# Kernel tuning notes

Measured on AMD Instinct MI355X. Metric: run time of the kernel, lower is better.

## Reference

```python
import jax, jax.numpy as jnp
import numpy as np

N_KNOTS = 10
NC = 32
BATCH = 32
EPS = 1e-5

def _spline_matrix(n):
    step = 1.0 / (n - 1.0)
    mat = 4 * np.eye(n - 2)
    np.fill_diagonal(mat[1:, :-1], 1)
    np.fill_diagonal(mat[:-1, 1:], 1)
    A = 6 * np.linalg.inv(mat) / step ** 2
    z = np.zeros(n - 2)
    A = np.vstack([z, A, z])            # [n, n-2]
    B = np.zeros((n - 2, n))
    np.fill_diagonal(B, 1)
    np.fill_diagonal(B[:, 1:], -2)
    np.fill_diagonal(B[:, 2:], 1)
    return np.dot(A, B).astype(np.float32)  # [n, n]

def setup_inputs() -> dict:
    key = jax.random.key(0)
    ks = jax.random.split(key, 8)
    n, nc = N_KNOTS, NC
    inp = {}
    inp['batch'] = jax.random.uniform(ks[0], (BATCH, 3, 256, 256), dtype=jnp.float32)
    chans = [3, nc, 2 * nc, 4 * nc, 8 * nc, 16 * nc]
    for i in range(5):
        ci, co = chans[i], chans[i + 1]
        inp['c%d_w' % (i + 1)] = jax.random.normal(jax.random.fold_in(ks[1], i), (co, ci, 3, 3), dtype=jnp.float32) * 0.1
        inp['c%d_b' % (i + 1)] = jnp.zeros((co,), jnp.float32)
        inp['bn%d_g' % (i + 1)] = jnp.ones((co,), jnp.float32)
        inp['bn%d_b' % (i + 1)] = jnp.zeros((co,), jnp.float32)
    inp['l1_w'] = jax.random.normal(ks[2], (100 * n, 16 * nc * 7 * 7), dtype=jnp.float32) * 0.02
    inp['l1_b'] = jnp.zeros((100 * n,), jnp.float32)
    inp['l2_w'] = jax.random.normal(ks[3], (3 * n, 100 * n), dtype=jnp.float32) * 0.02
    inp['l2_b'] = jnp.zeros((3 * n,), jnp.float32)
    inp['matrix'] = jnp.asarray(_spline_matrix(n))
    return inp

def _conv_bn(x, w, b, g, be):
    # conv (stride 2, VALID) -> relu -> batchnorm (training-mode batch stats)
    y = jax.lax.conv_general_dilated(x, w, (2, 2), 'VALID', dimension_numbers=('NCHW', 'OIHW', 'NCHW'))
    y = jax.nn.relu(y + b[None, :, None, None])
    m = jnp.mean(y, axis=(0, 2, 3))
    v = jnp.var(y, axis=(0, 2, 3))
    inv = jax.lax.rsqrt(v + EPS)
    return g[None, :, None, None] * (y - m[None, :, None, None]) * inv[None, :, None, None] + be[None, :, None, None]

def _forward(batch, c1_w, c1_b, bn1_g, bn1_b, c2_w, c2_b, bn2_g, bn2_b,
             c3_w, c3_b, bn3_g, bn3_b, c4_w, c4_b, bn4_g, bn4_b,
             c5_w, c5_b, bn5_g, bn5_b, l1_w, l1_b, l2_w, l2_b, matrix):
    n = matrix.shape[0]
    h = 1.0 / (n - 1.0)  # knot spacing (self.step)
    B, _, H, W = batch.shape

    x = _conv_bn(batch, c1_w, c1_b, bn1_g, bn1_b)
    x = _conv_bn(x, c2_w, c2_b, bn2_g, bn2_b)
    x = _conv_bn(x, c3_w, c3_b, bn3_g, bn3_b)
    x = _conv_bn(x, c4_w, c4_b, bn4_g, bn4_b)
    x = _conv_bn(x, c5_w, c5_b, bn5_g, bn5_b)
    x = x.reshape(B, -1)
    x = jax.nn.relu(x @ l1_w.T + l1_b)
    x = x @ l2_w.T + l2_b
    ys = x.reshape(B, 3, n) / 100.0

    identity = jnp.arange(n, dtype=batch.dtype) / (n - 1)
    ys_aug = ys + identity                                    # [B,3,n]
    # second-derivative values M at knots (natural cubic spline solve as dense matmul)
    M = jnp.einsum('ij,bcj->bci', matrix, ys_aug)             # [B,3,n]
    a = (M[..., 1:] - M[..., :-1]) / (6 * h)                  # [B,3,n-1]
    b_ = M[..., :-1] / 2
    c_ = (ys_aug[..., 1:] - ys_aug[..., :-1]) / h - (M[..., 1:] + 2 * M[..., :-1]) * (h / 6)
    d_ = ys_aug[..., :-1]

    def eval_spline(xv):  # xv: [B,3,K] -> [B,3,K]; gather segment coeffs instead of one-hot matmul
        xi = jnp.clip(jnp.floor(xv / h), 0, n - 2).astype(jnp.int32)
        xf = xv - xi.astype(xv.dtype) * h
        ag = jnp.take_along_axis(a, xi, axis=-1)
        bg = jnp.take_along_axis(b_, xi, axis=-1)
        cg = jnp.take_along_axis(c_, xi, axis=-1)
        dg = jnp.take_along_axis(d_, xi, axis=-1)
        return ((ag * xf + bg) * xf + cg) * xf + dg

    out = eval_spline(batch.reshape(B, 3, H * W)).reshape(B, 3, H, W)
    vals = jnp.arange(255, dtype=batch.dtype) / 255.0          # arange(0,1,1/255)
    splines = eval_spline(jnp.broadcast_to(vals, (B, 3, 255)))
    return out, splines

def reference(batch, c1_w, c1_b, bn1_g, bn1_b, c2_w, c2_b, bn2_g, bn2_b,
              c3_w, c3_b, bn3_g, bn3_b, c4_w, c4_b, bn4_g, bn4_b,
              c5_w, c5_b, bn5_g, bn5_b, l1_w, l1_b, l2_w, l2_b, matrix):
    return _forward(batch, c1_w, c1_b, bn1_g, bn1_b, c2_w, c2_b, bn2_g, bn2_b,
                    c3_w, c3_b, bn3_g, bn3_b, c4_w, c4_b, bn4_g, bn4_b,
                    c5_w, c5_b, bn5_g, bn5_b, l1_w, l1_b, l2_w, l2_b, matrix)
```

## Files before the change

kernel.cpp:

```cpp
#include <hip/hip_runtime.h>
#include <hip/hip_bf16.h>

#define BEPS 1e-5f
#define FC1_KS 98
#define FC1_KC 256
#define C1NB 2017

typedef __attribute__((ext_vector_type(8))) short short8v;
typedef __attribute__((ext_vector_type(4))) float f32x4;
typedef unsigned short ushort_t;

__device__ __forceinline__ float bf2f(ushort_t u) {
    unsigned int x = ((unsigned int)u) << 16;
    return __builtin_bit_cast(float, x);
}
__device__ __forceinline__ ushort_t f2bf(float v) {
    __hip_bfloat16 h = __float2bfloat16(v);
    return *(ushort_t*)&h;
}

__global__ __launch_bounds__(256) void conv1_direct(
    const float* __restrict__ in, const float* __restrict__ w,
    const float* __restrict__ bias, ushort_t* __restrict__ out,
    float* __restrict__ part) {
    __shared__ float ws[864];
    __shared__ float bs[32];
    __shared__ float tp[256 * 36];
    __shared__ float ps[8][32], pq[8][32];
    const int tid = threadIdx.x;
    for (int i = tid; i < 864; i += 256) ws[i] = w[i];
    if (tid < 32) bs[tid] = bias[tid];
    __syncthreads();

    const int TOT = 32 * 16129;
    int p = blockIdx.x * 256 + tid;
    const bool valid = (p < TOT);
    int pc = valid ? p : (TOT - 1);
    int b = pc / 16129, pp = pc - b * 16129;
    int i = pp / 127, j = pp - i * 127;
    const float* ib = in + ((long long)b * 3) * 65536 + (2 * i) * 256 + 2 * j;
    float patch[27];
#pragma unroll
    for (int ci = 0; ci < 3; ++ci)
#pragma unroll
        for (int di = 0; di < 3; ++di) {
            const float* rp = ib + ci * 65536 + di * 256;
            float2 v01 = *(const float2*)rp;
            patch[ci * 9 + di * 3 + 0] = v01.x;
            patch[ci * 9 + di * 3 + 1] = v01.y;
            patch[ci * 9 + di * 3 + 2] = rp[2];
        }

    float vals[32];
#pragma unroll
    for (int co = 0; co < 32; co += 4) {
        float a0 = bs[co], a1 = bs[co + 1], a2 = bs[co + 2], a3 = bs[co + 3];
#pragma unroll
        for (int t = 0; t < 27; ++t) {
            float pv = patch[t];
            a0 = fmaf(pv, ws[(co + 0) * 27 + t], a0);
            a1 = fmaf(pv, ws[(co + 1) * 27 + t], a1);
            a2 = fmaf(pv, ws[(co + 2) * 27 + t], a2);
            a3 = fmaf(pv, ws[(co + 3) * 27 + t], a3);
        }
        vals[co + 0] = fmaxf(a0, 0.f);
        vals[co + 1] = fmaxf(a1, 0.f);
        vals[co + 2] = fmaxf(a2, 0.f);
        vals[co + 3] = fmaxf(a3, 0.f);
    }
    if (valid) {
        ushort_t res[32];
#pragma unroll
        for (int c = 0; c < 32; ++c) res[c] = f2bf(vals[c]);
        ushort_t* ob = out + (long long)p * 32;
#pragma unroll
        for (int v = 0; v < 4; ++v)
            *(short8v*)&ob[v * 8] = *(const short8v*)&res[v * 8];
    } else {
#pragma unroll
        for (int c = 0; c < 32; ++c) vals[c] = 0.f;
    }
#pragma unroll
    for (int v = 0; v < 8; ++v)
        *(float4*)&tp[tid * 36 + v * 4] = make_float4(vals[v * 4], vals[v * 4 + 1],
                                                      vals[v * 4 + 2], vals[v * 4 + 3]);
    __syncthreads();
    {
        const int c = tid & 31, s = tid >> 5;
        float sm = 0.f, sq = 0.f;
#pragma unroll 8
        for (int q = 0; q < 32; ++q) {
            float v = tp[(s * 32 + q) * 36 + c];
            sm += v;
            sq = fmaf(v, v, sq);
        }
        ps[s][c] = sm;
        pq[s][c] = sq;
    }
    __syncthreads();
    if (tid < 32) {
        float sm = 0.f, sq = 0.f;
#pragma unroll
        for (int s = 0; s < 8; ++s) { sm += ps[s][tid]; sq += pq[s][tid]; }
        part[((long long)tid * C1NB + blockIdx.x) * 2 + 0] = sm;
        part[((long long)tid * C1NB + blockIdx.x) * 2 + 1] = sq;
    }
}

__global__ __launch_bounds__(512) void conv_mfma512(
    const ushort_t* __restrict__ in, const ushort_t* __restrict__ wf,
    const float* __restrict__ effb, ushort_t* __restrict__ out,
    float* __restrict__ spart,
    int B, int Ci, int lgCi, int Hi, int Wi, int Co, int Ho, int Wo,
    int K, int Kp, int kcount, int Spart) {
    const int HoWo = Ho * Wo;
    const int N = B * HoWo;
    __shared__ __align__(16) ushort_t As[64 * 64];
    __shared__ __align__(16) ushort_t Bs[256 * 64];
    const int tid = threadIdx.x;
    const int m0 = blockIdx.y * 64;
    const int n0 = blockIdx.x * 256;

    const int rowA = tid >> 3;
    const int kqA = (tid & 7) * 8;
    const ushort_t* wrowA = wf + (long long)(m0 + rowA) * Kp + kqA;
    const int swA = (rowA & 7) << 3;
    const int rowB = tid >> 1;
    const int kqB = (tid & 1) * 32;
    const int n = n0 + rowB;
    const int nn = (n < N) ? n : (N - 1);
    const int pb = nn / HoWo, pp = nn - pb * HoWo;
    const int pi = pp / Wo, pj = pp - pi * Wo;
    const long long base0 = ((long long)pb * Hi + 2 * pi) * Wi + 2 * pj;
    const int swB = (rowB & 7) << 3;

    const int w = tid >> 6;
    const int lane = tid & 63;
    const int wco = (w >> 2) * 32;
    const int wpx = (w & 3) * 64;
    const int lm = lane & 15, lk = lane >> 4;

    short8v rA0, rB[4];
    rA0 = *(const short8v*)(wrowA);
#pragma unroll
    for (int ch = 0; ch < 2; ++ch) {
        int c16 = kqB + ch * 16;
        int kg = c16;
        int tap = kg >> lgCi;
        tap = tap > 8 ? 8 : tap;
        int ci0 = kg & (Ci - 1);
        int dy = tap / 3, dx = tap - dy * 3;
        const ushort_t* src = in + (base0 + dy * Wi + dx) * Ci + ci0;
        rB[ch * 2] = *(const short8v*)src;
        rB[ch * 2 + 1] = *(const short8v*)(src + 8);
    }

    f32x4 acc[2][4] = {};
    for (int k0 = 0; k0 < kcount; k0 += 64) {
        *(short8v*)&As[rowA * 64 + (kqA ^ swA)] = rA0;
#pragma unroll
        for (int ch = 0; ch < 2; ++ch) {
            int c16 = kqB + ch * 16;
            *(short8v*)&Bs[rowB * 64 + ((c16 + 0) ^ swB)] = rB[ch * 2];
            *(short8v*)&Bs[rowB * 64 + ((c16 + 8) ^ swB)] = rB[ch * 2 + 1];
        }
        __syncthreads();
        int k1 = k0 + 64;
        if (k1 < kcount) {
            rA0 = *(const short8v*)(wrowA + k1);
#pragma unroll
            for (int ch = 0; ch < 2; ++ch) {
                int c16 = kqB + ch * 16;
                int kg = k1 + c16;
                int tap = kg >> lgCi;
                tap = tap > 8 ? 8 : tap;
                int ci0 = kg & (Ci - 1);
                int dy = tap / 3, dx = tap - dy * 3;
                const ushort_t* src = in + (base0 + dy * Wi + dx) * Ci + ci0;
                rB[ch * 2] = *(const short8v*)src;
                rB[ch * 2 + 1] = *(const short8v*)(src + 8);
            }
        }
#pragma unroll
        for (int kk = 0; kk < 2; ++kk) {
            const int kb = kk * 32 + lk * 8;
            const int ra0 = wco + lm, ra1 = wco + 16 + lm;
            short8v a0 = *(const short8v*)&As[ra0 * 64 + (kb ^ ((ra0 & 7) << 3))];
            short8v a1 = *(const short8v*)&As[ra1 * 64 + (kb ^ ((ra1 & 7) << 3))];
            const int rb0 = wpx + lm, rb1 = wpx + 16 + lm;
            const int rb2 = wpx + 32 + lm, rb3 = wpx + 48 + lm;
            short8v b0 = *(const short8v*)&Bs[rb0 * 64 + (kb ^ ((rb0 & 7) << 3))];
            short8v b1 = *(const short8v*)&Bs[rb1 * 64 + (kb ^ ((rb1 & 7) << 3))];
            short8v b2 = *(const short8v*)&Bs[rb2 * 64 + (kb ^ ((rb2 & 7) << 3))];
            short8v b3 = *(const short8v*)&Bs[rb3 * 64 + (kb ^ ((rb3 & 7) << 3))];
            acc[0][0] = __builtin_amdgcn_mfma_f32_16x16x32_bf16(a0, b0, acc[0][0], 0, 0, 0);
            acc[0][1] = __builtin_amdgcn_mfma_f32_16x16x32_bf16(a0, b1, acc[0][1], 0, 0, 0);
            acc[0][2] = __builtin_amdgcn_mfma_f32_16x16x32_bf16(a0, b2, acc[0][2], 0, 0, 0);
            acc[0][3] = __builtin_amdgcn_mfma_f32_16x16x32_bf16(a0, b3, acc[0][3], 0, 0, 0);
            acc[1][0] = __builtin_amdgcn_mfma_f32_16x16x32_bf16(a1, b0, acc[1][0], 0, 0, 0);
            acc[1][1] = __builtin_amdgcn_mfma_f32_16x16x32_bf16(a1, b1, acc[1][1], 0, 0, 0);
            acc[1][2] = __builtin_amdgcn_mfma_f32_16x16x32_bf16(a1, b2, acc[1][2], 0, 0, 0);
            acc[1][3] = __builtin_amdgcn_mfma_f32_16x16x32_bf16(a1, b3, acc[1][3], 0, 0, 0);
        }
        __syncthreads();
    }
    float ssum[2][4] = {}, ssq[2][4] = {};
#pragma unroll
    for (int nb = 0; nb < 4; ++nb) {
        int np = n0 + wpx + nb * 16 + lm;
        bool val = (np < N);
#pragma unroll
        for (int amr = 0; amr < 2; ++amr) {
            int cobase = m0 + wco + amr * 16 + lk * 4;
            float4 eb = *(const float4*)&effb[cobase];
            float v0 = fmaxf(acc[amr][nb][0] + eb.x, 0.f);
            float v1 = fmaxf(acc[amr][nb][1] + eb.y, 0.f);
            float v2 = fmaxf(acc[amr][nb][2] + eb.z, 0.f);
            float v3 = fmaxf(acc[amr][nb][3] + eb.w, 0.f);
            if (val) {
                ushort4 u;
                u.x = f2bf(v0); u.y = f2bf(v1); u.z = f2bf(v2); u.w = f2bf(v3);
                *(ushort4*)&out[(long long)np * Co + cobase] = u;
                ssum[amr][0] += v0; ssq[amr][0] = fmaf(v0, v0, ssq[amr][0]);
                ssum[amr][1] += v1; ssq[amr][1] = fmaf(v1, v1, ssq[amr][1]);
                ssum[amr][2] += v2; ssq[amr][2] = fmaf(v2, v2, ssq[amr][2]);
                ssum[amr][3] += v3; ssq[amr][3] = fmaf(v3, v3, ssq[amr][3]);
            }
        }
    }
#pragma unroll
    for (int mm = 1; mm < 16; mm <<= 1) {
#pragma unroll
        for (int amr = 0; amr < 2; ++amr)
#pragma unroll
            for (int r = 0; r < 4; ++r) {
                ssum[amr][r] += __shfl_xor(ssum[amr][r], mm, 64);
                ssq[amr][r] += __shfl_xor(ssq[amr][r], mm, 64);
            }
    }
    __shared__ float lss[8][32], lsq[8][32];
    if (lm == 0) {
#pragma unroll
        for (int amr = 0; amr < 2; ++amr)
#pragma unroll
            for (int r = 0; r < 4; ++r) {
                lss[w][amr * 16 + lk * 4 + r] = ssum[amr][r];
                lsq[w][amr * 16 + lk * 4 + r] = ssq[amr][r];
            }
    }
    __syncthreads();
    if (tid < 64) {
        int half = tid >> 5, c32 = tid & 31;
        float s = 0.f, q = 0.f;
#pragma unroll
        for (int qv = 0; qv < 4; ++qv) {
            s += lss[half * 4 + qv][c32];
            q += lsq[half * 4 + qv][c32];
        }
        int c = m0 + half * 32 + c32;
        spart[((long long)c * Spart + blockIdx.x) * 2 + 0] = s;
        spart[((long long)c * Spart + blockIdx.x) * 2 + 1] = q;
    }
}

__global__ __launch_bounds__(256) void conv_mfma(
    const ushort_t* __restrict__ in, const ushort_t* __restrict__ wf,
    const float* __restrict__ effb, ushort_t* __restrict__ out,
    float* __restrict__ pacc, float* __restrict__ spart,
    int B, int Ci, int lgCi, int Hi, int Wi, int Co, int Ho, int Wo,
    int K, int Kp, int kcount, int Spart) {
    const int HoWo = Ho * Wo;
    const int N = B * HoWo;
    __shared__ __align__(16) ushort_t As[64 * 64];
    __shared__ __align__(16) ushort_t Bs[128 * 64];
    const int tid = threadIdx.x;
    const int m0 = blockIdx.y * 64;
    const int n0 = blockIdx.x * 128;
    const int kbeg = blockIdx.z * kcount;

    const int rowA = tid >> 2;
    const int kqA = (tid & 3) * 16;
    const ushort_t* wrowA = wf + (long long)(m0 + rowA) * Kp + kbeg + kqA;
    const int swA = (rowA & 7) << 3;
    const int rowB = tid >> 1;
    const int kqB = (tid & 1) * 32;
    const int n = n0 + rowB;
    const int nn = (n < N) ? n : (N - 1);
    const int pb = nn / HoWo, pp = nn - pb * HoWo;
    const int pi = pp / Wo, pj = pp - pi * Wo;
    const long long base0 = ((long long)pb * Hi + 2 * pi) * Wi + 2 * pj;
    const int swB = (rowB & 7) << 3;

    const int w = tid >> 6;
    const int lane = tid & 63;
    const int wco = (w >> 1) * 32, wpx = (w & 1) * 64;
    const int lm = lane & 15, lk = lane >> 4;

    short8v rA0, rA1, rB[4];
    rA0 = *(const short8v*)(wrowA);
    rA1 = *(const short8v*)(wrowA + 8);
#pragma unroll
    for (int ch = 0; ch < 2; ++ch) {
        int c16 = kqB + ch * 16;
        int kg = kbeg + c16;
        int tap = kg >> lgCi;
        tap = tap > 8 ? 8 : tap;
        int ci0 = kg & (Ci - 1);
        int dy = tap / 3, dx = tap - dy * 3;
        const ushort_t* src = in + (base0 + dy * Wi + dx) * Ci + ci0;
        rB[ch * 2] = *(const short8v*)src;
        rB[ch * 2 + 1] = *(const short8v*)(src + 8);
    }

    f32x4 acc[2][4] = {};
    for (int k0 = 0; k0 < kcount; k0 += 64) {
        *(short8v*)&As[rowA * 64 + ((kqA + 0) ^ swA)] = rA0;
        *(short8v*)&As[rowA * 64 + ((kqA + 8) ^ swA)] = rA1;
#pragma unroll
        for (int ch = 0; ch < 2; ++ch) {
            int c16 = kqB + ch * 16;
            *(short8v*)&Bs[rowB * 64 + ((c16 + 0) ^ swB)] = rB[ch * 2];
            *(short8v*)&Bs[rowB * 64 + ((c16 + 8) ^ swB)] = rB[ch * 2 + 1];
        }
        __syncthreads();
        int k1 = k0 + 64;
        if (k1 < kcount) {
            rA0 = *(const short8v*)(wrowA + k1);
            rA1 = *(const short8v*)(wrowA + k1 + 8);
#pragma unroll
            for (int ch = 0; ch < 2; ++ch) {
                int c16 = kqB + ch * 16;
                int kg = kbeg + k1 + c16;
                int tap = kg >> lgCi;
                tap = tap > 8 ? 8 : tap;
                int ci0 = kg & (Ci - 1);
                int dy = tap / 3, dx = tap - dy * 3;
                const ushort_t* src = in + (base0 + dy * Wi + dx) * Ci + ci0;
                rB[ch * 2] = *(const short8v*)src;
                rB[ch * 2 + 1] = *(const short8v*)(src + 8);
            }
        }
#pragma unroll
        for (int kk = 0; kk < 2; ++kk) {
            const int kb = kk * 32 + lk * 8;
            const int ra0 = wco + lm, ra1 = wco + 16 + lm;
            short8v a0 = *(const short8v*)&As[ra0 * 64 + (kb ^ ((ra0 & 7) << 3))];
            short8v a1 = *(const short8v*)&As[ra1 * 64 + (kb ^ ((ra1 & 7) << 3))];
            const int rb0 = wpx + lm, rb1 = wpx + 16 + lm;
            const int rb2 = wpx + 32 + lm, rb3 = wpx + 48 + lm;
            short8v b0 = *(const short8v*)&Bs[rb0 * 64 + (kb ^ ((rb0 & 7) << 3))];
            short8v b1 = *(const short8v*)&Bs[rb1 * 64 + (kb ^ ((rb1 & 7) << 3))];
            short8v b2 = *(const short8v*)&Bs[rb2 * 64 + (kb ^ ((rb2 & 7) << 3))];
            short8v b3 = *(const short8v*)&Bs[rb3 * 64 + (kb ^ ((rb3 & 7) << 3))];
            acc[0][0] = __builtin_amdgcn_mfma_f32_16x16x32_bf16(a0, b0, acc[0][0], 0, 0, 0);
            acc[0][1] = __builtin_amdgcn_mfma_f32_16x16x32_bf16(a0, b1, acc[0][1], 0, 0, 0);
            acc[0][2] = __builtin_amdgcn_mfma_f32_16x16x32_bf16(a0, b2, acc[0][2], 0, 0, 0);
            acc[0][3] = __builtin_amdgcn_mfma_f32_16x16x32_bf16(a0, b3, acc[0][3], 0, 0, 0);
            acc[1][0] = __builtin_amdgcn_mfma_f32_16x16x32_bf16(a1, b0, acc[1][0], 0, 0, 0);
            acc[1][1] = __builtin_amdgcn_mfma_f32_16x16x32_bf16(a1, b1, acc[1][1], 0, 0, 0);
            acc[1][2] = __builtin_amdgcn_mfma_f32_16x16x32_bf16(a1, b2, acc[1][2], 0, 0, 0);
            acc[1][3] = __builtin_amdgcn_mfma_f32_16x16x32_bf16(a1, b3, acc[1][3], 0, 0, 0);
        }
        __syncthreads();
    }
    if (pacc) {
        float* pbuf = pacc + ((long long)blockIdx.z * N) * Co;
#pragma unroll
        for (int nb = 0; nb < 4; ++nb) {
            int np = n0 + wpx + nb * 16 + lm;
            if (np >= N) continue;
#pragma unroll
            for (int amr = 0; amr < 2; ++amr) {
                int cobase = m0 + wco + amr * 16 + lk * 4;
                float4 vv = make_float4(acc[amr][nb][0], acc[amr][nb][1],
                                        acc[amr][nb][2], acc[amr][nb][3]);
                *(float4*)&pbuf[(long long)np * Co + cobase] = vv;
            }
        }
    } else {
        float ssum[2][4] = {}, ssq[2][4] = {};
#pragma unroll
        for (int nb = 0; nb < 4; ++nb) {
            int np = n0 + wpx + nb * 16 + lm;
            bool val = (np < N);
#pragma unroll
            for (int amr = 0; amr < 2; ++amr) {
                int cobase = m0 + wco + amr * 16 + lk * 4;
                float4 eb = *(const float4*)&effb[cobase];
                float v0 = fmaxf(acc[amr][nb][0] + eb.x, 0.f);
                float v1 = fmaxf(acc[amr][nb][1] + eb.y, 0.f);
                float v2 = fmaxf(acc[amr][nb][2] + eb.z, 0.f);
                float v3 = fmaxf(acc[amr][nb][3] + eb.w, 0.f);
                if (val) {
                    ushort4 u;
                    u.x = f2bf(v0); u.y = f2bf(v1); u.z = f2bf(v2); u.w = f2bf(v3);
                    *(ushort4*)&out[(long long)np * Co + cobase] = u;
                    ssum[amr][0] += v0; ssq[amr][0] = fmaf(v0, v0, ssq[amr][0]);
                    ssum[amr][1] += v1; ssq[amr][1] = fmaf(v1, v1, ssq[amr][1]);
                    ssum[amr][2] += v2; ssq[amr][2] = fmaf(v2, v2, ssq[amr][2]);
                    ssum[amr][3] += v3; ssq[amr][3] = fmaf(v3, v3, ssq[amr][3]);
                }
            }
        }
#pragma unroll
        for (int mm = 1; mm < 16; mm <<= 1) {
#pragma unroll
            for (int amr = 0; amr < 2; ++amr)
#pragma unroll
                for (int r = 0; r < 4; ++r) {
                    ssum[amr][r] += __shfl_xor(ssum[amr][r], mm, 64);
                    ssq[amr][r] += __shfl_xor(ssq[amr][r], mm, 64);
                }
        }
        __shared__ float lss[4][32], lsq[4][32];
        if (lm == 0) {
#pragma unroll
            for (int amr = 0; amr < 2; ++amr)
#pragma unroll
                for (int r = 0; r < 4; ++r) {
                    lss[w][amr * 16 + lk * 4 + r] = ssum[amr][r];
                    lsq[w][amr * 16 + lk * 4 + r] = ssq[amr][r];
                }
        }
        __syncthreads();
        if (tid < 64) {
            int half = tid >> 5, c32 = tid & 31;
            float s = lss[half * 2][c32] + lss[half * 2 + 1][c32];
            float q = lsq[half * 2][c32] + lsq[half * 2 + 1][c32];
            int c = m0 + half * 32 + c32;
            spart[((long long)c * Spart + blockIdx.x) * 2 + 0] = s;
            spart[((long long)c * Spart + blockIdx.x) * 2 + 1] = q;
        }
    }
}

__global__ __launch_bounds__(256) void convz_stats(
    const float* __restrict__ pacc, const float* __restrict__ effb,
    ushort_t* __restrict__ out, float* __restrict__ part,
    long long total, int Co, int Z) {
    const int tid = threadIdx.x;
    const int c0 = (tid * 8) & (Co - 1);
    float eb[8];
    {
        float4 e0 = *(const float4*)&effb[c0];
        float4 e1 = *(const float4*)&effb[c0 + 4];
        eb[0] = e0.x; eb[1] = e0.y; eb[2] = e0.z; eb[3] = e0.w;
        eb[4] = e1.x; eb[5] = e1.y; eb[6] = e1.z; eb[7] = e1.w;
    }
    float sum[8] = {}, sq[8] = {};
    const long long nchunk = total >> 11;
    for (long long g = blockIdx.x; g < nchunk; g += 512) {
        long long off = (g << 11) + tid * 8;
        float v[8];
#pragma unroll
        for (int j = 0; j < 8; ++j) v[j] = eb[j];
        for (int z = 0; z < Z; ++z) {
            const float* pz = pacc + (long long)z * total + off;
            float4 a = *(const float4*)pz;
            float4 b2 = *(const float4*)(pz + 4);
            v[0] += a.x; v[1] += a.y; v[2] += a.z; v[3] += a.w;
            v[4] += b2.x; v[5] += b2.y; v[6] += b2.z; v[7] += b2.w;
        }
        short8v o;
#pragma unroll
        for (int j = 0; j < 8; ++j) {
            float r = fmaxf(v[j], 0.f);
            o[j] = (short)f2bf(r);
            sum[j] += r;
            sq[j] = fmaf(r, r, sq[j]);
        }
        *(short8v*)&out[off] = o;
    }
    __shared__ float rs[256][8], rq[256][8];
#pragma unroll
    for (int j = 0; j < 8; ++j) { rs[tid][j] = sum[j]; rq[tid][j] = sq[j]; }
    __syncthreads();
    const int G = Co >> 3;
    const int TPG = 256 / G;
    for (int c = tid; c < Co; c += 256) {
        int grp = c >> 3, j = c & 7;
        float s = 0.f, q = 0.f;
        for (int i = 0; i < TPG; ++i) {
            s += rs[grp + i * G][j];
            q += rq[grp + i * G][j];
        }
        part[(c * 512 + blockIdx.x) * 2 + 0] = s;
        part[(c * 512 + blockIdx.x) * 2 + 1] = q;
    }
}

__global__ __launch_bounds__(256) void stats_final_w(
    const float* __restrict__ part, const float* __restrict__ g,
    const float* __restrict__ be, float* __restrict__ scale,
    float* __restrict__ shift, int C, int S, float invN) {
    int c = blockIdx.x * 4 + (threadIdx.x >> 6);
    int lane = threadIdx.x & 63;
    if (c >= C) return;
    float s = 0.f, q = 0.f;
    for (int i = lane; i < S; i += 64) {
        s += part[((long long)c * S + i) * 2 + 0];
        q += part[((long long)c * S + i) * 2 + 1];
    }
#pragma unroll
    for (int off = 32; off > 0; off >>= 1) {
        s += __shfl_down(s, off, 64);
        q += __shfl_down(q, off, 64);
    }
    if (lane == 0) {
        float m = s * invN;
        float v = q * invN - m * m;
        float inv = rsqrtf(v + BEPS);
        float sc = g[c] * inv;
        scale[c] = sc;
        shift[c] = be[c] - m * sc;
    }
}

__global__ __launch_bounds__(256) void fold_fused(
    const float* __restrict__ w, const float* __restrict__ scale,
    const float* __restrict__ shift, const float* __restrict__ bias,
    ushort_t* __restrict__ wout, float* __restrict__ effb,
    int Ci, int lgCi, int K, int Kp, int Co, int WB) {
    if ((int)blockIdx.x < WB) {
        int idx = blockIdx.x * 256 + threadIdx.x;
        if (idx >= Co * Kp) return;
        int co = idx / Kp, k = idx - co * Kp;
        ushort_t o = 0;
        if (k < K) {
            int tap = k >> lgCi;
            int ci = k & (Ci - 1);
            o = f2bf(w[((long long)co * Ci + ci) * 9 + tap] * scale[ci]);
        }
        wout[idx] = o;
    } else {
        int co = ((int)blockIdx.x - WB) * 4 + (threadIdx.x >> 6);
        int lane = threadIdx.x & 63;
        if (co >= Co) return;
        const int CK = Ci * 9;
        const float* wr = w + (long long)co * CK;
        float acc = 0.f;
        for (int k = lane; k < CK; k += 64) acc = fmaf(wr[k], shift[k / 9], acc);
#pragma unroll
        for (int off = 32; off > 0; off >>= 1) acc += __shfl_down(acc, off, 64);
        if (lane == 0) effb[co] = acc + bias[co];
    }
}

__global__ void bn_apply_x(const ushort_t* __restrict__ y, const float* __restrict__ scale,
                           const float* __restrict__ shift, ushort_t* __restrict__ xB) {
    int idx = blockIdx.x * blockDim.x + threadIdx.x;
    if (idx >= 802816) return;
    int b = idx / 25088, k = idx - b * 25088;
    int c = k / 49, p = k - c * 49;
    float v = bf2f(y[((long long)b * 49 + p) * 512 + c]);
    xB[idx] = f2bf(fmaf(v, scale[c], shift[c]));
}

__global__ __launch_bounds__(256) void fc1_mfma(
    const float* __restrict__ w, const ushort_t* __restrict__ xB,
    float* __restrict__ part) {
    const int K = 25088;
    __shared__ __align__(16) ushort_t As[64 * 256];
    __shared__ __align__(16) ushort_t Bs[32 * 256];
    const int tid = threadIdx.x;
    const int m0 = blockIdx.y * 64;
    const int kbeg = blockIdx.x * FC1_KC;

    {
        const int r = tid >> 2;
        const int kq = (tid & 3) * 64;
        const int m = m0 + r;
        const bool mv = (m < 1000);
        const float* wr = w + (long long)m * K + kbeg + kq;
        const int sw = (r & 7) << 3;
#pragma unroll
        for (int g = 0; g < 8; ++g) {
            short8v o = {0, 0, 0, 0, 0, 0, 0, 0};
            if (mv) {
                float4 f0 = *(const float4*)(wr + g * 8);
                float4 f1 = *(const float4*)(wr + g * 8 + 4);
                o[0] = (short)f2bf(f0.x); o[1] = (short)f2bf(f0.y);
                o[2] = (short)f2bf(f0.z); o[3] = (short)f2bf(f0.w);
                o[4] = (short)f2bf(f1.x); o[5] = (short)f2bf(f1.y);
                o[6] = (short)f2bf(f1.z); o[7] = (short)f2bf(f1.w);
            }
            *(short8v*)&As[r * 256 + ((kq + g * 8) ^ sw)] = o;
        }
    }
    {
        const int b = tid >> 3;
        const int kq = (tid & 7) * 32;
        const ushort_t* xr = xB + (long long)b * K + kbeg + kq;
        const int sw = (b & 7) << 3;
#pragma unroll
        for (int g = 0; g < 4; ++g) {
            short8v v = *(const short8v*)(xr + g * 8);
            *(short8v*)&Bs[b * 256 + ((kq + g * 8) ^ sw)] = v;
        }
    }
    __syncthreads();
    const int wv = tid >> 6, lane = tid & 63;
    const int lm = lane & 15, lk = lane >> 4;
    const int wm = wv * 16;
    f32x4 acc0 = {}, acc1 = {};
    const int ra = wm + lm;
    const int swa = (ra & 7) << 3;
    const int swb = (lm & 7) << 3;
#pragma unroll
    for (int s = 0; s < 8; ++s) {
        int kb = s * 32 + lk * 8;
        short8v av = *(const short8v*)&As[ra * 256 + (kb ^ swa)];
        short8v b0 = *(const short8v*)&Bs[lm * 256 + (kb ^ swb)];
        short8v b1 = *(const short8v*)&Bs[(16 + lm) * 256 + (kb ^ swb)];
        acc0 = __builtin_amdgcn_mfma_f32_16x16x32_bf16(av, b0, acc0, 0, 0, 0);
        acc1 = __builtin_amdgcn_mfma_f32_16x16x32_bf16(av, b1, acc1, 0, 0, 0);
    }
    float* pb = part + ((long long)blockIdx.y * FC1_KS + blockIdx.x) * 2048;
#pragma unroll
    for (int r = 0; r < 4; ++r) {
        pb[(wm + lk * 4 + r) * 32 + lm] = acc0[r];
        pb[(wm + lk * 4 + r) * 32 + 16 + lm] = acc1[r];
    }
}

__global__ void fc1_reduce(const float* __restrict__ part, const float* __restrict__ bias,
                           float* __restrict__ z) {
    int idx = blockIdx.x * blockDim.x + threadIdx.x;
    if (idx >= 32000) return;
    int o = idx >> 5, b = idx & 31;
    int mt = o >> 6, mr = o & 63;
    const float* p = part + ((long long)mt * FC1_KS) * 2048 + mr * 32 + b;
    float s0 = 0.f, s1 = 0.f;
    int ks = 0;
    for (; ks + 1 < FC1_KS; ks += 2) {
        s0 += p[(long long)ks * 2048];
        s1 += p[(long long)(ks + 1) * 2048];
    }
    for (; ks < FC1_KS; ++ks) s0 += p[(long long)ks * 2048];
    z[b * 1000 + o] = fmaxf(s0 + s1 + bias[o], 0.f);
}

__global__ __launch_bounds__(256) void fc2_v2(const float* __restrict__ z,
                                              const float* __restrict__ w,
                                              const float* __restrict__ bias,
                                              float* __restrict__ ys) {
    int gid = blockIdx.x * 4 + (threadIdx.x >> 6);
    int lane = threadIdx.x & 63;
    if (gid >= 960) return;
    int b = gid / 30, o = gid - b * 30;
    const float* zr = z + (long long)b * 1000;
    const float* wr = w + (long long)o * 1000;
    float acc = 0.f;
    for (int k = lane; k < 1000; k += 64) acc = fmaf(zr[k], wr[k], acc);
    for (int off = 32; off > 0; off >>= 1) acc += __shfl_down(acc, off, 64);
    if (lane == 0) ys[gid] = acc + bias[o];
}

__global__ __launch_bounds__(256) void eval_all(
    const float4* __restrict__ batch4, const float* __restrict__ ysraw,
    const float* __restrict__ matrix, float4* __restrict__ out4,
    float* __restrict__ outt) {
    __shared__ float mat[100];
    __shared__ float4 coefs[864];
    const int tid = threadIdx.x;
    const float h = 1.0f / 9.0f;
    if (tid < 100) mat[tid] = matrix[tid];
    __syncthreads();
    if (tid < 96) {
        int b = tid / 3, ch = tid - b * 3;
        float ya[10];
#pragma unroll
        for (int j = 0; j < 10; ++j)
            ya[j] = ysraw[b * 30 + ch * 10 + j] / 100.0f + (float)j / 9.0f;
        float M[10];
#pragma unroll
        for (int i = 0; i < 10; ++i) {
            float acc = 0.f;
#pragma unroll
            for (int j = 0; j < 10; ++j) acc = fmaf(mat[i * 10 + j], ya[j], acc);
            M[i] = acc;
        }
#pragma unroll
        for (int k = 0; k < 9; ++k) {
            float a = (M[k + 1] - M[k]) / (6.0f * h);
            float bb = M[k] * 0.5f;
            float cc = (ya[k + 1] - ya[k]) / h - (M[k + 1] + 2.0f * M[k]) * (h / 6.0f);
            float dd = ya[k];
            coefs[tid * 9 + k] = make_float4(a, bb, cc, dd);
        }
    }
    __syncthreads();
    int idx = blockIdx.x * 256 + tid;
    if (idx < 1572864) {
        int plane = idx >> 14;
        float4 xv4 = batch4[idx];
        float xin[4] = {xv4.x, xv4.y, xv4.z, xv4.w};
        float xout[4];
#pragma unroll
        for (int e = 0; e < 4; ++e) {
            float xv = xin[e];
            int xi = (int)floorf(xv / h);
            xi = min(max(xi, 0), 8);
            float xf = xv - (float)xi * h;
            float4 cf = coefs[plane * 9 + xi];
            xout[e] = fmaf(fmaf(fmaf(cf.x, xf, cf.y), xf, cf.z), xf, cf.w);
        }
        out4[idx] = make_float4(xout[0], xout[1], xout[2], xout[3]);
    } else {
        int t = idx - 1572864;
        if (t < 96 * 255) {
            int plane = t / 255;
            int j = t - plane * 255;
            float xv = (float)j / 255.0f;
            int xi = (int)floorf(xv / h);
            xi = min(max(xi, 0), 8);
            float xf = xv - (float)xi * h;
            float4 cf = coefs[plane * 9 + xi];
            outt[t] = fmaf(fmaf(fmaf(cf.x, xf, cf.y), xf, cf.z), xf, cf.w);
        }
    }
}

extern "C" void kernel_launch(void* const* d_in, const int* in_sizes, int n_in,
                              void* d_out, int out_size, void* d_ws, size_t ws_size,
                              hipStream_t stream) {
    const int B = 32;
    const float* batch = (const float*)d_in[0];
    const float* cw[5] = {(const float*)d_in[1], (const float*)d_in[5], (const float*)d_in[9],
                          (const float*)d_in[13], (const float*)d_in[17]};
    const float* cb[5] = {(const float*)d_in[2], (const float*)d_in[6], (const float*)d_in[10],
                          (const float*)d_in[14], (const float*)d_in[18]};
    const float* bg[5] = {(const float*)d_in[3], (const float*)d_in[7], (const float*)d_in[11],
                          (const float*)d_in[15], (const float*)d_in[19]};
    const float* bb[5] = {(const float*)d_in[4], (const float*)d_in[8], (const float*)d_in[12],
                          (const float*)d_in[16], (const float*)d_in[20]};
    const float* l1w = (const float*)d_in[21];
    const float* l1b = (const float*)d_in[22];
    const float* l2w = (const float*)d_in[23];
    const float* l2b = (const float*)d_in[24];
    const float* matrix = (const float*)d_in[25];

    float* f = (float*)d_ws;
    const size_t A_F = 8258048;
    const size_t Bq_F = 4064256;
    const size_t W_F = 589824;
    ushort_t* bufA = (ushort_t*)f;
    ushort_t* bufB = (ushort_t*)(f + A_F);
    ushort_t* Wf_bf = (ushort_t*)(f + A_F + Bq_F);
    float* effb  = f + A_F + Bq_F + W_F;
    float* scale = effb + 512;
    float* shift = scale + 512;
    float* part  = shift + 512;
    float* x5    = part + 524288;
    float* pacc  = x5 + 802816;
    float* z1    = pacc + 3686400;
    float* ysb   = z1 + 32000;

    const int Ci[5]   = {3, 32, 64, 128, 256};
    const int lgCi[5] = {0, 5, 6, 7, 8};
    const int Co[5]   = {32, 64, 128, 256, 512};
    const int Hi[5]   = {256, 127, 63, 31, 15};
    const int Ho[5]   = {127, 63, 31, 15, 7};
    const int Zl[5]   = {1, 1, 1, 1, 3};

    ushort_t* bufs[2] = {bufA, bufB};

    conv1_direct<<<C1NB, 256, 0, stream>>>(batch, cw[0], cb[0], bufA, part);
    stats_final_w<<<8, 256, 0, stream>>>(part, bg[0], bb[0], scale, shift, 32, C1NB,
                                         1.0f / (float)(B * 16129));

    const ushort_t* cur = bufA;
    for (int l = 1; l < 5; ++l) {
        ushort_t* outb = bufs[l % 2];
        int K = Ci[l] * 9;
        int Kp = (K + 63) & ~63;
        int WB = (Co[l] * Kp + 255) / 256;
        int BBk = (Co[l] + 3) / 4;
        fold_fused<<<WB + BBk, 256, 0, stream>>>(cw[l], scale, shift, cb[l], Wf_bf, effb,
                                                 Ci[l], lgCi[l], K, Kp, Co[l], WB);
        int N = B * Ho[l] * Ho[l];
        int Z = Zl[l];
        int kcount = Kp / Z;
        if (l <= 2) {
            dim3 grid((N + 255) / 256, Co[l] / 64, 1);
            conv_mfma512<<<grid, 512, 0, stream>>>(cur, Wf_bf, effb, outb, part,
                                                   B, Ci[l], lgCi[l], Hi[l], Hi[l], Co[l],
                                                   Ho[l], Ho[l], K, Kp, Kp, grid.x);
            stats_final_w<<<(Co[l] + 3) / 4, 256, 0, stream>>>(
                part, bg[l], bb[l], scale, shift, Co[l], grid.x, 1.0f / (float)N);
        } else if (Z == 1) {
            dim3 grid((N + 127) / 128, Co[l] / 64, 1);
            conv_mfma<<<grid, 256, 0, stream>>>(cur, Wf_bf, effb, outb, nullptr, part,
                                                B, Ci[l], lgCi[l], Hi[l], Hi[l], Co[l],
                                                Ho[l], Ho[l], K, Kp, kcount, grid.x);
            stats_final_w<<<(Co[l] + 3) / 4, 256, 0, stream>>>(
                part, bg[l], bb[l], scale, shift, Co[l], grid.x, 1.0f / (float)N);
        } else {
            dim3 grid((N + 127) / 128, Co[l] / 64, Z);
            conv_mfma<<<grid, 256, 0, stream>>>(cur, Wf_bf, effb, nullptr, pacc, nullptr,
                                                B, Ci[l], lgCi[l], Hi[l], Hi[l], Co[l],
                                                Ho[l], Ho[l], K, Kp, kcount, 0);
            long long total = (long long)N * Co[l];
            convz_stats<<<512, 256, 0, stream>>>(pacc, effb, outb, part, total, Co[l], Z);
            stats_final_w<<<(Co[l] + 3) / 4, 256, 0, stream>>>(
                part, bg[l], bb[l], scale, shift, Co[l], 512, 1.0f / (float)N);
        }
        cur = outb;
    }

    ushort_t* xB = (ushort_t*)x5;
    bn_apply_x<<<(802816 + 255) / 256, 256, 0, stream>>>(cur, scale, shift, xB);
    {
        dim3 grid(FC1_KS, 16);
        fc1_mfma<<<grid, 256, 0, stream>>>(l1w, xB, pacc);
    }
    fc1_reduce<<<(32000 + 255) / 256, 256, 0, stream>>>(pacc, l1b, z1);
    fc2_v2<<<240, 256, 0, stream>>>(z1, l2w, l2b, ysb);

    float* out = (float*)d_out;
    int evtot = 1572864 + 96 * 255;
    eval_all<<<(evtot + 255) / 256, 256, 0, stream>>>((const float4*)batch, ysb, matrix,
                                                      (float4*)out, out + 6291456);
}
```

Baseline: 236.0 us.

## Fuse layer-5 BN finalize and apply into fc1 MFMA B-tile load

Each fc1 block now reduces the layer-5 per-channel sum and sum-of-squares partials for the up to 8 channels it touches, then builds scale and shift in shared memory. It applies batch norm while gathering the bf16 conv output straight into the B tile, so the separate bn_apply_x pass and the last stats_final_w launch are removed, along with the transposed activation buffer. The cost is redundant stats reduction in every block and strided, uncoalesced gathers from the NHWC conv output. The stats_final_w call is also dropped from the whole split-K branch, which is only correct if that branch runs only for the last layer.

```diff
diff --git a/kernel.cpp b/kernel.cpp
--- a/kernel.cpp
+++ b/kernel.cpp
@@ -546,26 +546,43 @@
     }
 }
 
-__global__ void bn_apply_x(const ushort_t* __restrict__ y, const float* __restrict__ scale,
-                           const float* __restrict__ shift, ushort_t* __restrict__ xB) {
-    int idx = blockIdx.x * blockDim.x + threadIdx.x;
-    if (idx >= 802816) return;
-    int b = idx / 25088, k = idx - b * 25088;
-    int c = k / 49, p = k - c * 49;
-    float v = bf2f(y[((long long)b * 49 + p) * 512 + c]);
-    xB[idx] = f2bf(fmaf(v, scale[c], shift[c]));
-}
-
 __global__ __launch_bounds__(256) void fc1_mfma(
-    const float* __restrict__ w, const ushort_t* __restrict__ xB,
-    float* __restrict__ part) {
+    const float* __restrict__ w, const ushort_t* __restrict__ y5,
+    const float* __restrict__ part, const float* __restrict__ g5,
+    const float* __restrict__ be5, float* __restrict__ partout) {
     const int K = 25088;
     __shared__ __align__(16) ushort_t As[64 * 256];
     __shared__ __align__(16) ushort_t Bs[32 * 256];
+    __shared__ float sc_s[8], sh_s[8];
     const int tid = threadIdx.x;
     const int m0 = blockIdx.y * 64;
     const int kbeg = blockIdx.x * FC1_KC;
-
+    const int cbase = kbeg / 49;
+
+    {
+        int cl = tid >> 5, i0 = tid & 31;
+        int c = cbase + cl;
+        if (c > 511) c = 511;
+        float s = 0.f, q = 0.f;
+        for (int i = i0; i < 512; i += 32) {
+            s += part[((long long)c * 512 + i) * 2 + 0];
+            q += part[((long long)c * 512 + i) * 2 + 1];
+        }
+#pragma unroll
+        for (int off = 16; off > 0; off >>= 1) {
+            s += __shfl_down(s, off, 32);
+            q += __shfl_down(q, off, 32);
+        }
+        if (i0 == 0) {
+            const float invN = 1.0f / 1568.0f;
+            float m = s * invN;
+            float v = q * invN - m * m;
+            float inv = rsqrtf(v + BEPS);
+            float sc = g5[c] * inv;
+            sc_s[cl] = sc;
+            sh_s[cl] = be5[c] - m * sc;
+        }
+    }
     {
         const int r = tid >> 2;
         const int kq = (tid & 3) * 64;
@@ -574,28 +591,38 @@
         const float* wr = w + (long long)m * K + kbeg + kq;
         const int sw = (r & 7) << 3;
 #pragma unroll
-        for (int g = 0; g < 8; ++g) {
+        for (int gg = 0; gg < 8; ++gg) {
             short8v o = {0, 0, 0, 0, 0, 0, 0, 0};
             if (mv) {
-                float4 f0 = *(const float4*)(wr + g * 8);
-                float4 f1 = *(const float4*)(wr + g * 8 + 4);
+                float4 f0 = *(const float4*)(wr + gg * 8);
+                float4 f1 = *(const float4*)(wr + gg * 8 + 4);
                 o[0] = (short)f2bf(f0.x); o[1] = (short)f2bf(f0.y);
                 o[2] = (short)f2bf(f0.z); o[3] = (short)f2bf(f0.w);
                 o[4] = (short)f2bf(f1.x); o[5] = (short)f2bf(f1.y);
                 o[6] = (short)f2bf(f1.z); o[7] = (short)f2bf(f1.w);
             }
-            *(short8v*)&As[r * 256 + ((kq + g * 8) ^ sw)] = o;
-        }
-    }
+            *(short8v*)&As[r * 256 + ((kq + gg * 8) ^ sw)] = o;
+        }
+    }
+    __syncthreads();
     {
         const int b = tid >> 3;
         const int kq = (tid & 7) * 32;
-        const ushort_t* xr = xB + (long long)b * K + kbeg + kq;
         const int sw = (b & 7) << 3;
-#pragma unroll
-        for (int g = 0; g < 4; ++g) {
-            short8v v = *(const short8v*)(xr + g * 8);
-            *(short8v*)&Bs[b * 256 + ((kq + g * 8) ^ sw)] = v;
+        const long long ybase = (long long)b * 49 * 512;
+#pragma unroll
+        for (int gg = 0; gg < 4; ++gg) {
+            short8v v;
+#pragma unroll
+            for (int e = 0; e < 8; ++e) {
+                int k = kbeg + kq + gg * 8 + e;
+                int c = k / 49;
+                int p = k - c * 49;
+                float xv = bf2f(y5[ybase + (long long)p * 512 + c]);
+                float r = fmaf(xv, sc_s[c - cbase], sh_s[c - cbase]);
+                v[e] = (short)f2bf(r);
+            }
+            *(short8v*)&Bs[b * 256 + ((kq + gg * 8) ^ sw)] = v;
         }
     }
     __syncthreads();
@@ -615,7 +642,7 @@
         acc0 = __builtin_amdgcn_mfma_f32_16x16x32_bf16(av, b0, acc0, 0, 0, 0);
         acc1 = __builtin_amdgcn_mfma_f32_16x16x32_bf16(av, b1, acc1, 0, 0, 0);
     }
-    float* pb = part + ((long long)blockIdx.y * FC1_KS + blockIdx.x) * 2048;
+    float* pb = partout + ((long long)blockIdx.y * FC1_KS + blockIdx.x) * 2048;
 #pragma unroll
     for (int r = 0; r < 4; ++r) {
         pb[(wm + lk * 4 + r) * 32 + lm] = acc0[r];
@@ -802,17 +829,13 @@
                                                 Ho[l], Ho[l], K, Kp, kcount, 0);
             long long total = (long long)N * Co[l];
             convz_stats<<<512, 256, 0, stream>>>(pacc, effb, outb, part, total, Co[l], Z);
-            stats_final_w<<<(Co[l] + 3) / 4, 256, 0, stream>>>(
-                part, bg[l], bb[l], scale, shift, Co[l], 512, 1.0f / (float)N);
         }
         cur = outb;
     }
 
-    ushort_t* xB = (ushort_t*)x5;
-    bn_apply_x<<<(802816 + 255) / 256, 256, 0, stream>>>(cur, scale, shift, xB);
     {
         dim3 grid(FC1_KS, 16);
-        fc1_mfma<<<grid, 256, 0, stream>>>(l1w, xB, pacc);
+        fc1_mfma<<<grid, 256, 0, stream>>>(l1w, cur, part, bg[4], bb[4], pacc);
     }
     fc1_reduce<<<(32000 + 255) / 256, 256, 0, stream>>>(pacc, l1b, z1);
     fc2_v2<<<240, 256, 0, stream>>>(z1, l2w, l2b, ysb);
```

New measurement: 277.2 us. 17.5% more time.
